# Optimization experiments

Hardware: AMD Instinct MI355X
Metric: run time of the kernel (lower is better)

## Reference

```python
import jax, jax.numpy as jnp
import numpy as np

B, CK, CQ, CV, CO, H, W = 4, 256, 256, 256, 64, 24, 24


def setup_inputs() -> dict:
    key = jax.random.key(0)
    ks = jax.random.split(key, 9)
    s = lambda k, shape, fan: jax.random.normal(k, shape, jnp.float32) * (fan ** -0.5)
    return {
        "key": jax.random.normal(ks[0], (B, CK, H, W), jnp.float32),
        "query": jax.random.normal(ks[1], (B, CQ, H, W), jnp.float32),
        "value": jax.random.normal(ks[2], (B, CV, H, W), jnp.float32),
        "Wk": s(ks[3], (CO, CK), CK),   # 1x1 conv weight for key transform
        "bk": jnp.zeros((CO,), jnp.float32),
        "Wq": s(ks[4], (CO, CQ), CQ),   # 1x1 conv weight for query transform
        "bq": jnp.zeros((CO,), jnp.float32),
        "wf": s(ks[5], (CO,), CO),      # channel-flattening 1x1 conv (CO -> 1)
        "bf": jnp.zeros((), jnp.float32),
    }


def reference(key, query, value, Wk, bk, Wq, bq, wf, bf):
    b, _, hq, wq = query.shape
    nk = key.shape[2] * key.shape[3]
    nq = hq * wq
    # 1x1 conv == per-pixel linear; flatten spatial to (B, N, CO)
    k_ = jnp.einsum('bchw,oc->bhwo', key, Wk).reshape(b, nk, -1) + bk
    q_ = jnp.einsum('bchw,oc->bhwo', query, Wq).reshape(b, nq, -1) + bq
    # broadcast add: (B, Nk, 1, CO) + (B, 1, Nq, CO) -> tanh -> reduce channels
    pre = jnp.tanh(k_[:, :, None, :] + q_[:, None, :, :])
    scores = jnp.einsum('bkqc,c->bkq', pre, wf) + bf
    attn = jax.nn.sigmoid(scores)                      # (B, Nk, Nq)
    v_ = value.reshape(b, value.shape[1], nk)          # (B, CV, Nk)
    out = jnp.einsum('bkq,bck->bcq', attn, v_)         # (B, CV, Nq)
    return out.reshape(b, value.shape[1], hq, wq)
```

## Files before the change

### kernel.cpp

```cpp
#include <hip/hip_runtime.h>
#include <hip/hip_bf16.h>

#define BB 4
#define CIN 256
#define CO 64
#define NN 576
#define NKC 18
#define NMT 36
#define NQT 36

typedef __attribute__((ext_vector_type(8))) short short8;
typedef __attribute__((ext_vector_type(4))) float floatx4;

__device__ __forceinline__ unsigned short f2bf(float f) {
    unsigned int u = __float_as_uint(f);
    unsigned int r = (u + 0x7fffu + ((u >> 16) & 1u)) >> 16;
    return (unsigned short)r;
}

__global__ void __launch_bounds__(256) pack_all(
    const float* __restrict__ key, const float* __restrict__ query,
    const float* __restrict__ value,
    const float* __restrict__ Wk, const float* __restrict__ Wq,
    unsigned short* __restrict__ Xp, unsigned short* __restrict__ Wp,
    unsigned short* __restrict__ Vp)
{
    __shared__ float tile[32][33];
    int bid = blockIdx.x;
    int t = threadIdx.x;
    int l = t & 63;
    int w = t >> 6;

    if (bid < 1152) {
        int zb  = bid / 144;
        int r   = bid % 144;
        int n32 = r % 18;
        int kc  = r / 18;
        int z = zb >> 2, b = zb & 3;
        const float* src = z ? query : key;
        int tx = t & 31, ty = t >> 5;
        const float* s = src + ((size_t)b * CIN + (size_t)kc * 32) * NN + n32 * 32;
        #pragma unroll
        for (int j = 0; j < 4; ++j) {
            int cl = ty + j * 8;
            tile[cl][tx] = s[(size_t)cl * NN + tx];
        }
        __syncthreads();
        if (w < 2) {
            int nl = w * 16 + (l & 15);
            int cl = (l >> 4) * 8;
            uint4 o;
            o.x = (unsigned)f2bf(tile[cl + 0][nl]) | ((unsigned)f2bf(tile[cl + 1][nl]) << 16);
            o.y = (unsigned)f2bf(tile[cl + 2][nl]) | ((unsigned)f2bf(tile[cl + 3][nl]) << 16);
            o.z = (unsigned)f2bf(tile[cl + 4][nl]) | ((unsigned)f2bf(tile[cl + 5][nl]) << 16);
            o.w = (unsigned)f2bf(tile[cl + 6][nl]) | ((unsigned)f2bf(tile[cl + 7][nl]) << 16);
            int mt = n32 * 2 + w;
            *(uint4*)(Xp + ((((size_t)z * BB + b) * NMT + mt) * 8 + kc) * 512 + l * 8) = o;
        }
    } else if (bid < 1168) {
        int funit = (bid - 1152) * 4 + w;
        int z  = funit >> 5;
        int nt = (funit >> 3) & 3;
        int kc = funit & 7;
        const float* W = z ? Wq : Wk;
        int o = nt * 16 + (l & 15);
        int c = kc * 32 + (l >> 4) * 8;
        const float4* p = (const float4*)(W + (size_t)o * CIN + c);
        float4 v0 = p[0], v1 = p[1];
        uint4 u;
        u.x = (unsigned)f2bf(v0.x) | ((unsigned)f2bf(v0.y) << 16);
        u.y = (unsigned)f2bf(v0.z) | ((unsigned)f2bf(v0.w) << 16);
        u.z = (unsigned)f2bf(v1.x) | ((unsigned)f2bf(v1.y) << 16);
        u.w = (unsigned)f2bf(v1.z) | ((unsigned)f2bf(v1.w) << 16);
        *(uint4*)(Wp + (((size_t)z * 4 + nt) * 8 + kc) * 512 + l * 8) = u;
    } else {
        int funit = (bid - 1168) * 4 + w;
        int b  = funit / 288;
        int r  = funit % 288;
        int ct = r / 18;
        int kc = r % 18;
        int c = ct * 16 + (l & 15);
        int k = kc * 32 + (l >> 4) * 8;
        const float4* p = (const float4*)(value + ((size_t)b * CIN + c) * NN + k);
        float4 v0 = p[0], v1 = p[1];
        uint4 u;
        u.x = (unsigned)f2bf(v0.x) | ((unsigned)f2bf(v0.y) << 16);
        u.y = (unsigned)f2bf(v0.z) | ((unsigned)f2bf(v0.w) << 16);
        u.z = (unsigned)f2bf(v1.x) | ((unsigned)f2bf(v1.y) << 16);
        u.w = (unsigned)f2bf(v1.z) | ((unsigned)f2bf(v1.w) << 16);
        *(uint4*)(Vp + (((size_t)b * 16 + ct) * NKC + kc) * 512 + l * 8) = u;
    }
}

__global__ void __launch_bounds__(256) proj_exp_mfma(
    const unsigned short* __restrict__ Xp, const unsigned short* __restrict__ Wp,
    const float* __restrict__ bk, const float* __restrict__ bq,
    float* __restrict__ ek, float* __restrict__ eq)
{
    int t = threadIdx.x, l = t & 63, w = t >> 6;
    int gw = blockIdx.x * 4 + w;
    int z  = gw / 144;
    int r  = gw % 144;
    int b  = r / NMT;
    int mt = r % NMT;

    const unsigned short* ab = Xp + ((((size_t)z * BB + b) * NMT + mt) * 8) * 512 + l * 8;
    const unsigned short* wb = Wp + (size_t)z * 32 * 512 + l * 8;

    floatx4 acc[4] = {{0.f,0.f,0.f,0.f},{0.f,0.f,0.f,0.f},
                      {0.f,0.f,0.f,0.f},{0.f,0.f,0.f,0.f}};
    #pragma unroll
    for (int kc = 0; kc < 8; ++kc) {
        short8 a = *(const short8*)(ab + (size_t)kc * 512);
        #pragma unroll
        for (int nt = 0; nt < 4; ++nt) {
            short8 bf8 = *(const short8*)(wb + ((size_t)nt * 8 + kc) * 512);
            acc[nt] = __builtin_amdgcn_mfma_f32_16x16x32_bf16(a, bf8, acc[nt], 0, 0, 0);
        }
    }

    const float* bias = z ? bq : bk;
    float* outp       = z ? eq : ek;
    int n0 = mt * 16;
    #pragma unroll
    for (int nt = 0; nt < 4; ++nt) {
        int o = nt * 16 + (l & 15);
        float bv = bias[o];
        #pragma unroll
        for (int rr = 0; rr < 4; ++rr) {
            int row = (l >> 4) * 4 + rr;
            outp[((size_t)b * NN + n0 + row) * CO + o] = __expf(2.0f * (acc[nt][rr] + bv));
        }
    }
}

__global__ void __launch_bounds__(256, 3) attn_pack_kernel(
    const float* __restrict__ ek, const float* __restrict__ eq,
    const float* __restrict__ wf, const float* __restrict__ bfp,
    unsigned short* __restrict__ Bp)
{
    int b  = blockIdx.z;
    int k0 = blockIdx.y * 32;
    int q0 = blockIdx.x * 64;
    int t  = threadIdx.x;
    int l  = t & 63;
    int w  = __builtin_amdgcn_readfirstlane(t >> 6);

    __shared__ float eqs[64 * 65];
    __shared__ float sc[32 * 65];

    const float4* esrc = (const float4*)(eq + ((size_t)b * NN + q0) * CO);
    #pragma unroll
    for (int i = 0; i < 4; ++i) {
        int f4  = t + i * 256;
        int row = f4 >> 4, c4 = (f4 & 15) * 4;
        float4 v = esrc[f4];
        int a = row * 65 + c4;
        eqs[a + 0] = v.x; eqs[a + 1] = v.y; eqs[a + 2] = v.z; eqs[a + 3] = v.w;
    }

    float4 w2v[16];
    float C = bfp[0];
    const float4* wfp4 = (const float4*)wf;
    #pragma unroll
    for (int i = 0; i < 16; ++i) {
        float4 wv = wfp4[i];
        C += wv.x + wv.y + wv.z + wv.w;
        wv.x *= 2.0f; wv.y *= 2.0f; wv.z *= 2.0f; wv.w *= 2.0f;
        w2v[i] = wv;
    }
    __syncthreads();

    float4 eqv[16];
    #pragma unroll
    for (int i = 0; i < 16; ++i) {
        int a = l * 65 + i * 4;
        eqv[i].x = eqs[a]; eqv[i].y = eqs[a + 1];
        eqv[i].z = eqs[a + 2]; eqv[i].w = eqs[a + 3];
    }

    #pragma unroll 1
    for (int kk = 0; kk < 8; ++kk) {
        int k = k0 + w * 8 + kk;
        const float4* ekr = (const float4*)(ek + ((size_t)b * NN + k) * CO);
        float a0 = 0.f, a1 = 0.f, a2 = 0.f, a3 = 0.f;
        #pragma unroll
        for (int i = 0; i < 16; ++i) {
            float4 k4 = ekr[i];
            float4 e4 = eqv[i];
            float4 w4 = w2v[i];
            a0 = fmaf(w4.x, __builtin_amdgcn_rcpf(fmaf(k4.x, e4.x, 1.0f)), a0);
            a1 = fmaf(w4.y, __builtin_amdgcn_rcpf(fmaf(k4.y, e4.y, 1.0f)), a1);
            a2 = fmaf(w4.z, __builtin_amdgcn_rcpf(fmaf(k4.z, e4.z, 1.0f)), a2);
            a3 = fmaf(w4.w, __builtin_amdgcn_rcpf(fmaf(k4.w, e4.w, 1.0f)), a3);
        }
        float score = C - (a0 + a1) - (a2 + a3);
        float sg = __builtin_amdgcn_rcpf(1.0f + __expf(-score));
        sc[(w * 8 + kk) * 65 + l] = sg;
    }
    __syncthreads();

    int col = w * 16 + (l & 15);
    int row = (l >> 4) * 8;
    uint4 o;
    o.x = (unsigned)f2bf(sc[(row + 0) * 65 + col]) | ((unsigned)f2bf(sc[(row + 1) * 65 + col]) << 16);
    o.y = (unsigned)f2bf(sc[(row + 2) * 65 + col]) | ((unsigned)f2bf(sc[(row + 3) * 65 + col]) << 16);
    o.z = (unsigned)f2bf(sc[(row + 4) * 65 + col]) | ((unsigned)f2bf(sc[(row + 5) * 65 + col]) << 16);
    o.w = (unsigned)f2bf(sc[(row + 6) * 65 + col]) | ((unsigned)f2bf(sc[(row + 7) * 65 + col]) << 16);
    size_t qt = (size_t)blockIdx.x * 4 + w;
    *(uint4*)(Bp + (((size_t)b * NQT + qt) * NKC + blockIdx.y) * 512 + l * 8) = o;
}

__global__ void __launch_bounds__(256) av_mfma_kernel(
    const unsigned short* __restrict__ Vp,
    const unsigned short* __restrict__ Bp,
    float* __restrict__ out)
{
    int b  = blockIdx.z;
    int ct = blockIdx.y;
    int qx = blockIdx.x;
    int t  = threadIdx.x;
    int l  = t & 63;
    int w  = __builtin_amdgcn_readfirstlane(t >> 6);

    floatx4 acc[4] = {{0.f,0.f,0.f,0.f},{0.f,0.f,0.f,0.f},
                      {0.f,0.f,0.f,0.f},{0.f,0.f,0.f,0.f}};

    const unsigned short* abase = Vp + ((size_t)b * 16 + ct) * NKC * 512 + l * 8;
    const unsigned short* bbase = Bp + ((size_t)b * NQT + (size_t)qx * 4) * NKC * 512 + l * 8;

    for (int kc = w; kc < NKC; kc += 4) {
        short8 a = *(const short8*)(abase + (size_t)kc * 512);
        #pragma unroll
        for (int qt = 0; qt < 4; ++qt) {
            short8 bq = *(const short8*)(bbase + ((size_t)qt * NKC + kc) * 512);
            acc[qt] = __builtin_amdgcn_mfma_f32_16x16x32_bf16(a, bq, acc[qt], 0, 0, 0);
        }
    }

    __shared__ float red[4][64][17];
    #pragma unroll
    for (int qt = 0; qt < 4; ++qt)
        #pragma unroll
        for (int r = 0; r < 4; ++r)
            red[w][l][qt * 4 + r] = acc[qt][r];
    __syncthreads();

    int q = qx * 64 + w * 16 + (l & 15);
    #pragma unroll
    for (int r = 0; r < 4; ++r) {
        float s = red[0][l][w * 4 + r] + red[1][l][w * 4 + r]
                + red[2][l][w * 4 + r] + red[3][l][w * 4 + r];
        int c = ct * 16 + (l >> 4) * 4 + r;
        out[((size_t)b * CIN + c) * NN + q] = s;
    }
}

extern "C" void kernel_launch(void* const* d_in, const int* in_sizes, int n_in,
                              void* d_out, int out_size, void* d_ws, size_t ws_size,
                              hipStream_t stream) {
    const float* key   = (const float*)d_in[0];
    const float* query = (const float*)d_in[1];
    const float* value = (const float*)d_in[2];
    const float* Wk    = (const float*)d_in[3];
    const float* bk    = (const float*)d_in[4];
    const float* Wq    = (const float*)d_in[5];
    const float* bq    = (const float*)d_in[6];
    const float* wf    = (const float*)d_in[7];
    const float* bf    = (const float*)d_in[8];
    float* out = (float*)d_out;

    float* ws = (float*)d_ws;
    float* ek = ws;
    float* eq = ek + (size_t)BB * NN * CO;
    unsigned short* Xp = (unsigned short*)(eq + (size_t)BB * NN * CO);
    unsigned short* Wp = Xp + (size_t)2 * BB * NMT * 8 * 512;
    unsigned short* Vp = Wp + (size_t)2 * 4 * 8 * 512;
    unsigned short* Bp = Vp + (size_t)BB * 16 * NKC * 512;

    pack_all<<<1456, 256, 0, stream>>>(key, query, value, Wk, Wq, Xp, Wp, Vp);

    proj_exp_mfma<<<72, 256, 0, stream>>>(Xp, Wp, bk, bq, ek, eq);

    dim3 ga(NN / 64, NN / 32, BB);
    attn_pack_kernel<<<ga, 256, 0, stream>>>(ek, eq, wf, bf, Bp);

    dim3 gm(NN / 64, 16, BB);
    av_mfma_kernel<<<gm, 256, 0, stream>>>(Vp, Bp, out);
}
```

Baseline: 102.3 us.

## Fuse input packing into projection MFMA kernel and stage ek tile in LDS

Merges the packing kernel and the projection MFMA kernel into one prep kernel. Each block now computes a 16-pixel projection tile directly from fp32 inputs, splitting K across four waves and reducing through LDS, which removes the bf16 Xp/Wp staging buffers and one launch. The attention kernel now stages its ek rows and the doubled wf weights in LDS and computes the bias constant with a wave reduction instead of per-thread register arrays, and its occupancy hint rises from 3 to 4 blocks. In exchange the prep kernel reads the weights redundantly per block, and the attention kernel uses more shared memory.

```diff
diff --git a/kernel.cpp b/kernel.cpp
--- a/kernel.cpp
+++ b/kernel.cpp
@@ -6,7 +6,6 @@
 #define CO 64
 #define NN 576
 #define NKC 18
-#define NMT 36
 #define NQT 36
 
 typedef __attribute__((ext_vector_type(8))) short short8;
@@ -18,67 +17,92 @@
     return (unsigned short)r;
 }
 
-__global__ void __launch_bounds__(256) pack_all(
+__global__ void __launch_bounds__(256) prep_kernel(
     const float* __restrict__ key, const float* __restrict__ query,
     const float* __restrict__ value,
     const float* __restrict__ Wk, const float* __restrict__ Wq,
-    unsigned short* __restrict__ Xp, unsigned short* __restrict__ Wp,
+    const float* __restrict__ bk, const float* __restrict__ bq,
+    float* __restrict__ ek, float* __restrict__ eq,
     unsigned short* __restrict__ Vp)
 {
-    __shared__ float tile[32][33];
+    __shared__ float red[4][4][64][4];
+    __shared__ float ex[16 * 69];
+
     int bid = blockIdx.x;
     int t = threadIdx.x;
     int l = t & 63;
-    int w = t >> 6;
-
-    if (bid < 1152) {
-        int zb  = bid / 144;
-        int r   = bid % 144;
-        int n32 = r % 18;
-        int kc  = r / 18;
-        int z = zb >> 2, b = zb & 3;
-        const float* src = z ? query : key;
-        int tx = t & 31, ty = t >> 5;
-        const float* s = src + ((size_t)b * CIN + (size_t)kc * 32) * NN + n32 * 32;
-        #pragma unroll
-        for (int j = 0; j < 4; ++j) {
-            int cl = ty + j * 8;
-            tile[cl][tx] = s[(size_t)cl * NN + tx];
-        }
+    int w = __builtin_amdgcn_readfirstlane(t >> 6);
+
+    if (bid < 288) {
+        int z  = bid / 144;
+        int r  = bid % 144;
+        int b  = r / 36;
+        int nt = r % 36;
+        int n0 = nt * 16;
+        const float* x = z ? query : key;
+        const float* W = z ? Wq : Wk;
+
+        floatx4 acc[4] = {{0.f,0.f,0.f,0.f},{0.f,0.f,0.f,0.f},
+                          {0.f,0.f,0.f,0.f},{0.f,0.f,0.f,0.f}};
+
+        #pragma unroll
+        for (int kci = 0; kci < 2; ++kci) {
+            int kc = w + kci * 4;
+            int cbase = kc * 32 + (l >> 4) * 8;
+            const float* xp = x + ((size_t)b * CIN + cbase) * NN + n0 + (l & 15);
+            uint4 bu;
+            {
+                float x0 = xp[0 * NN], x1 = xp[1 * NN], x2 = xp[2 * NN], x3 = xp[3 * NN];
+                float x4 = xp[4 * NN], x5 = xp[5 * NN], x6 = xp[6 * NN], x7 = xp[7 * NN];
+                bu.x = (unsigned)f2bf(x0) | ((unsigned)f2bf(x1) << 16);
+                bu.y = (unsigned)f2bf(x2) | ((unsigned)f2bf(x3) << 16);
+                bu.z = (unsigned)f2bf(x4) | ((unsigned)f2bf(x5) << 16);
+                bu.w = (unsigned)f2bf(x6) | ((unsigned)f2bf(x7) << 16);
+            }
+            short8 bx = *(short8*)&bu;
+            #pragma unroll
+            for (int mt = 0; mt < 4; ++mt) {
+                const float4* wp = (const float4*)(W + (size_t)(mt * 16 + (l & 15)) * CIN + cbase);
+                float4 w0 = wp[0], w1 = wp[1];
+                uint4 au;
+                au.x = (unsigned)f2bf(w0.x) | ((unsigned)f2bf(w0.y) << 16);
+                au.y = (unsigned)f2bf(w0.z) | ((unsigned)f2bf(w0.w) << 16);
+                au.z = (unsigned)f2bf(w1.x) | ((unsigned)f2bf(w1.y) << 16);
+                au.w = (unsigned)f2bf(w1.z) | ((unsigned)f2bf(w1.w) << 16);
+                acc[mt] = __builtin_amdgcn_mfma_f32_16x16x32_bf16(*(short8*)&au, bx, acc[mt], 0, 0, 0);
+            }
+        }
+        #pragma unroll
+        for (int mt = 0; mt < 4; ++mt)
+            #pragma unroll
+            for (int rr = 0; rr < 4; ++rr)
+                red[w][mt][l][rr] = acc[mt][rr];
         __syncthreads();
-        if (w < 2) {
-            int nl = w * 16 + (l & 15);
-            int cl = (l >> 4) * 8;
-            uint4 o;
-            o.x = (unsigned)f2bf(tile[cl + 0][nl]) | ((unsigned)f2bf(tile[cl + 1][nl]) << 16);
-            o.y = (unsigned)f2bf(tile[cl + 2][nl]) | ((unsigned)f2bf(tile[cl + 3][nl]) << 16);
-            o.z = (unsigned)f2bf(tile[cl + 4][nl]) | ((unsigned)f2bf(tile[cl + 5][nl]) << 16);
-            o.w = (unsigned)f2bf(tile[cl + 6][nl]) | ((unsigned)f2bf(tile[cl + 7][nl]) << 16);
-            int mt = n32 * 2 + w;
-            *(uint4*)(Xp + ((((size_t)z * BB + b) * NMT + mt) * 8 + kc) * 512 + l * 8) = o;
-        }
-    } else if (bid < 1168) {
-        int funit = (bid - 1152) * 4 + w;
-        int z  = funit >> 5;
-        int nt = (funit >> 3) & 3;
-        int kc = funit & 7;
-        const float* W = z ? Wq : Wk;
-        int o = nt * 16 + (l & 15);
-        int c = kc * 32 + (l >> 4) * 8;
-        const float4* p = (const float4*)(W + (size_t)o * CIN + c);
-        float4 v0 = p[0], v1 = p[1];
-        uint4 u;
-        u.x = (unsigned)f2bf(v0.x) | ((unsigned)f2bf(v0.y) << 16);
-        u.y = (unsigned)f2bf(v0.z) | ((unsigned)f2bf(v0.w) << 16);
-        u.z = (unsigned)f2bf(v1.x) | ((unsigned)f2bf(v1.y) << 16);
-        u.w = (unsigned)f2bf(v1.z) | ((unsigned)f2bf(v1.w) << 16);
-        *(uint4*)(Wp + (((size_t)z * 4 + nt) * 8 + kc) * 512 + l * 8) = u;
+
+        const float* bias = z ? bq : bk;
+        #pragma unroll
+        for (int rr = 0; rr < 4; ++rr) {
+            float v = red[0][w][l][rr] + red[1][w][l][rr]
+                    + red[2][w][l][rr] + red[3][w][l][rr];
+            int o = w * 16 + (l >> 4) * 4 + rr;
+            ex[(l & 15) * 69 + o] = __expf(2.0f * (v + bias[o]));
+        }
+        __syncthreads();
+
+        float* outp = z ? eq : ek;
+        float* obase = outp + ((size_t)b * NN + n0) * CO;
+        #pragma unroll
+        for (int i = 0; i < 4; ++i) {
+            int idx = t + i * 256;
+            int n = idx >> 6, o = idx & 63;
+            obase[(size_t)n * CO + o] = ex[n * 69 + o];
+        }
     } else {
-        int funit = (bid - 1168) * 4 + w;
+        int funit = (bid - 288) * 4 + w;
         int b  = funit / 288;
-        int r  = funit % 288;
-        int ct = r / 18;
-        int kc = r % 18;
+        int r2 = funit % 288;
+        int ct = r2 / NKC;
+        int kc = r2 % NKC;
         int c = ct * 16 + (l & 15);
         int k = kc * 32 + (l >> 4) * 8;
         const float4* p = (const float4*)(value + ((size_t)b * CIN + c) * NN + k);
@@ -92,49 +116,7 @@
     }
 }
 
-__global__ void __launch_bounds__(256) proj_exp_mfma(
-    const unsigned short* __restrict__ Xp, const unsigned short* __restrict__ Wp,
-    const float* __restrict__ bk, const float* __restrict__ bq,
-    float* __restrict__ ek, float* __restrict__ eq)
-{
-    int t = threadIdx.x, l = t & 63, w = t >> 6;
-    int gw = blockIdx.x * 4 + w;
-    int z  = gw / 144;
-    int r  = gw % 144;
-    int b  = r / NMT;
-    int mt = r % NMT;
-
-    const unsigned short* ab = Xp + ((((size_t)z * BB + b) * NMT + mt) * 8) * 512 + l * 8;
-    const unsigned short* wb = Wp + (size_t)z * 32 * 512 + l * 8;
-
-    floatx4 acc[4] = {{0.f,0.f,0.f,0.f},{0.f,0.f,0.f,0.f},
-                      {0.f,0.f,0.f,0.f},{0.f,0.f,0.f,0.f}};
-    #pragma unroll
-    for (int kc = 0; kc < 8; ++kc) {
-        short8 a = *(const short8*)(ab + (size_t)kc * 512);
-        #pragma unroll
-        for (int nt = 0; nt < 4; ++nt) {
-            short8 bf8 = *(const short8*)(wb + ((size_t)nt * 8 + kc) * 512);
-            acc[nt] = __builtin_amdgcn_mfma_f32_16x16x32_bf16(a, bf8, acc[nt], 0, 0, 0);
-        }
-    }
-
-    const float* bias = z ? bq : bk;
-    float* outp       = z ? eq : ek;
-    int n0 = mt * 16;
-    #pragma unroll
-    for (int nt = 0; nt < 4; ++nt) {
-        int o = nt * 16 + (l & 15);
-        float bv = bias[o];
-        #pragma unroll
-        for (int rr = 0; rr < 4; ++rr) {
-            int row = (l >> 4) * 4 + rr;
-            outp[((size_t)b * NN + n0 + row) * CO + o] = __expf(2.0f * (acc[nt][rr] + bv));
-        }
-    }
-}
-
-__global__ void __launch_bounds__(256, 3) attn_pack_kernel(
+__global__ void __launch_bounds__(256, 4) attn_pack_kernel(
     const float* __restrict__ ek, const float* __restrict__ eq,
     const float* __restrict__ wf, const float* __restrict__ bfp,
     unsigned short* __restrict__ Bp)
@@ -147,30 +129,37 @@
     int w  = __builtin_amdgcn_readfirstlane(t >> 6);
 
     __shared__ float eqs[64 * 65];
+    __shared__ float eks[32 * 68];
+    __shared__ float w2s[64];
+    __shared__ float Cs;
     __shared__ float sc[32 * 65];
 
     const float4* esrc = (const float4*)(eq + ((size_t)b * NN + q0) * CO);
     #pragma unroll
     for (int i = 0; i < 4; ++i) {
-        int f4  = t + i * 256;
+        int f4 = t + i * 256;
         int row = f4 >> 4, c4 = (f4 & 15) * 4;
         float4 v = esrc[f4];
         int a = row * 65 + c4;
-        eqs[a + 0] = v.x; eqs[a + 1] = v.y; eqs[a + 2] = v.z; eqs[a + 3] = v.w;
-    }
-
-    float4 w2v[16];
-    float C = bfp[0];
-    const float4* wfp4 = (const float4*)wf;
-    #pragma unroll
-    for (int i = 0; i < 16; ++i) {
-        float4 wv = wfp4[i];
-        C += wv.x + wv.y + wv.z + wv.w;
-        wv.x *= 2.0f; wv.y *= 2.0f; wv.z *= 2.0f; wv.w *= 2.0f;
-        w2v[i] = wv;
+        eqs[a] = v.x; eqs[a + 1] = v.y; eqs[a + 2] = v.z; eqs[a + 3] = v.w;
+    }
+    const float4* ksrc = (const float4*)(ek + ((size_t)b * NN + k0) * CO);
+    #pragma unroll
+    for (int i = 0; i < 2; ++i) {
+        int f4 = t + i * 256;
+        int row = f4 >> 4, c4 = (f4 & 15) * 4;
+        *(float4*)&eks[row * 68 + c4] = ksrc[f4];
+    }
+    if (t < 64) {
+        float v = wf[t];
+        w2s[t] = 2.0f * v;
+        #pragma unroll
+        for (int s = 32; s; s >>= 1) v += __shfl_xor(v, s, 64);
+        if (t == 0) Cs = v + bfp[0];
     }
     __syncthreads();
 
+    float C = Cs;
     float4 eqv[16];
     #pragma unroll
     for (int i = 0; i < 16; ++i) {
@@ -181,14 +170,14 @@
 
     #pragma unroll 1
     for (int kk = 0; kk < 8; ++kk) {
-        int k = k0 + w * 8 + kk;
-        const float4* ekr = (const float4*)(ek + ((size_t)b * NN + k) * CO);
+        int krow = w * 8 + kk;
+        const float* ekr = &eks[krow * 68];
         float a0 = 0.f, a1 = 0.f, a2 = 0.f, a3 = 0.f;
         #pragma unroll
         for (int i = 0; i < 16; ++i) {
-            float4 k4 = ekr[i];
+            float4 k4 = *(const float4*)(ekr + i * 4);
+            float4 w4 = *(const float4*)&w2s[i * 4];
             float4 e4 = eqv[i];
-            float4 w4 = w2v[i];
             a0 = fmaf(w4.x, __builtin_amdgcn_rcpf(fmaf(k4.x, e4.x, 1.0f)), a0);
             a1 = fmaf(w4.y, __builtin_amdgcn_rcpf(fmaf(k4.y, e4.y, 1.0f)), a1);
             a2 = fmaf(w4.z, __builtin_amdgcn_rcpf(fmaf(k4.z, e4.z, 1.0f)), a2);
@@ -196,7 +185,7 @@
         }
         float score = C - (a0 + a1) - (a2 + a3);
         float sg = __builtin_amdgcn_rcpf(1.0f + __expf(-score));
-        sc[(w * 8 + kk) * 65 + l] = sg;
+        sc[krow * 65 + l] = sg;
     }
     __syncthreads();
 
@@ -273,14 +262,10 @@
     float* ws = (float*)d_ws;
     float* ek = ws;
     float* eq = ek + (size_t)BB * NN * CO;
-    unsigned short* Xp = (unsigned short*)(eq + (size_t)BB * NN * CO);
-    unsigned short* Wp = Xp + (size_t)2 * BB * NMT * 8 * 512;
-    unsigned short* Vp = Wp + (size_t)2 * 4 * 8 * 512;
+    unsigned short* Vp = (unsigned short*)(eq + (size_t)BB * NN * CO);
     unsigned short* Bp = Vp + (size_t)BB * 16 * NKC * 512;
 
-    pack_all<<<1456, 256, 0, stream>>>(key, query, value, Wk, Wq, Xp, Wp, Vp);
-
-    proj_exp_mfma<<<72, 256, 0, stream>>>(Xp, Wp, bk, bq, ek, eq);
+    prep_kernel<<<576, 256, 0, stream>>>(key, query, value, Wk, Wq, bk, bq, ek, eq, Vp);
 
     dim3 ga(NN / 64, NN / 32, BB);
     attn_pack_kernel<<<ga, 256, 0, stream>>>(ek, eq, wf, bf, Bp);
```

New measurement: 174.4 us. +70.4%, slower.

## Stage ek tile and wf in LDS, widen pack tiles, split projection to one wave per block

Applied to the files above, without the earlier changes.

The attention kernel now loads its 32 ek rows and the doubled wf weights into shared memory once per block, and computes the wf sum with a wave shuffle reduction. Previously each wave read ek rows straight from global memory inside the inner loop and every thread kept wf in 16 float4 registers. The pack kernel transposes 64x32 tiles with all four waves writing output, where before it used 32x32 tiles with only two of four waves writing, so far fewer blocks are launched. The projection kernel runs one 64-thread wave per block over 288 blocks, spreading the work across more CUs. The extra LDS use in the attention kernel could lower occupancy, and reading w2s from LDS adds LDS traffic in the hot loop.

```diff
diff --git a/kernel.cpp b/kernel.cpp
--- a/kernel.cpp
+++ b/kernel.cpp
@@ -18,47 +18,58 @@
     return (unsigned short)r;
 }
 
-__global__ void __launch_bounds__(256) pack_all(
+__global__ void __launch_bounds__(256) pack_kernel(
     const float* __restrict__ key, const float* __restrict__ query,
     const float* __restrict__ value,
     const float* __restrict__ Wk, const float* __restrict__ Wq,
     unsigned short* __restrict__ Xp, unsigned short* __restrict__ Wp,
     unsigned short* __restrict__ Vp)
 {
-    __shared__ float tile[32][33];
+    __shared__ float tile[64 * 33];
     int bid = blockIdx.x;
-    int t = threadIdx.x;
-    int l = t & 63;
-    int w = t >> 6;
-
-    if (bid < 1152) {
-        int zb  = bid / 144;
-        int r   = bid % 144;
-        int n32 = r % 18;
-        int kc  = r / 18;
-        int z = zb >> 2, b = zb & 3;
-        const float* src = z ? query : key;
-        int tx = t & 31, ty = t >> 5;
-        const float* s = src + ((size_t)b * CIN + (size_t)kc * 32) * NN + n32 * 32;
-        #pragma unroll
-        for (int j = 0; j < 4; ++j) {
-            int cl = ty + j * 8;
-            tile[cl][tx] = s[(size_t)cl * NN + tx];
+    int t = threadIdx.x, l = t & 63, w = t >> 6;
+
+    if (bid < 576) {
+        int z = bid / 288, rem = bid % 288;
+        int b = rem / 72, rem2 = rem % 72;
+        int n32 = rem2 / 4, c64 = rem2 % 4;
+        const float* x = z ? query : key;
+        const float* s = x + ((size_t)b * CIN + c64 * 64) * NN + n32 * 32;
+        #pragma unroll
+        for (int j = 0; j < 8; ++j) {
+            int row = (t >> 5) + j * 8;
+            tile[row * 33 + (t & 31)] = s[(size_t)row * NN + (t & 31)];
         }
         __syncthreads();
-        if (w < 2) {
-            int nl = w * 16 + (l & 15);
-            int cl = (l >> 4) * 8;
-            uint4 o;
-            o.x = (unsigned)f2bf(tile[cl + 0][nl]) | ((unsigned)f2bf(tile[cl + 1][nl]) << 16);
-            o.y = (unsigned)f2bf(tile[cl + 2][nl]) | ((unsigned)f2bf(tile[cl + 3][nl]) << 16);
-            o.z = (unsigned)f2bf(tile[cl + 4][nl]) | ((unsigned)f2bf(tile[cl + 5][nl]) << 16);
-            o.w = (unsigned)f2bf(tile[cl + 6][nl]) | ((unsigned)f2bf(tile[cl + 7][nl]) << 16);
-            int mt = n32 * 2 + w;
-            *(uint4*)(Xp + ((((size_t)z * BB + b) * NMT + mt) * 8 + kc) * 512 + l * 8) = o;
-        }
-    } else if (bid < 1168) {
-        int funit = (bid - 1152) * 4 + w;
+        int mtl = w & 1, kcl = w >> 1;
+        int nl = mtl * 16 + (l & 15);
+        int cl = kcl * 32 + (l >> 4) * 8;
+        uint4 o;
+        o.x = (unsigned)f2bf(tile[(cl + 0) * 33 + nl]) | ((unsigned)f2bf(tile[(cl + 1) * 33 + nl]) << 16);
+        o.y = (unsigned)f2bf(tile[(cl + 2) * 33 + nl]) | ((unsigned)f2bf(tile[(cl + 3) * 33 + nl]) << 16);
+        o.z = (unsigned)f2bf(tile[(cl + 4) * 33 + nl]) | ((unsigned)f2bf(tile[(cl + 5) * 33 + nl]) << 16);
+        o.w = (unsigned)f2bf(tile[(cl + 6) * 33 + nl]) | ((unsigned)f2bf(tile[(cl + 7) * 33 + nl]) << 16);
+        int mt = n32 * 2 + mtl;
+        int kc = c64 * 2 + kcl;
+        *(uint4*)(Xp + ((((size_t)z * BB + b) * NMT + mt) * 8 + kc) * 512 + l * 8) = o;
+    } else if (bid < 864) {
+        int funit = (bid - 576) * 4 + w;
+        int b  = funit / 288;
+        int r2 = funit % 288;
+        int ct = r2 / NKC;
+        int kc = r2 % NKC;
+        int c = ct * 16 + (l & 15);
+        int k = kc * 32 + (l >> 4) * 8;
+        const float4* p = (const float4*)(value + ((size_t)b * CIN + c) * NN + k);
+        float4 v0 = p[0], v1 = p[1];
+        uint4 u;
+        u.x = (unsigned)f2bf(v0.x) | ((unsigned)f2bf(v0.y) << 16);
+        u.y = (unsigned)f2bf(v0.z) | ((unsigned)f2bf(v0.w) << 16);
+        u.z = (unsigned)f2bf(v1.x) | ((unsigned)f2bf(v1.y) << 16);
+        u.w = (unsigned)f2bf(v1.z) | ((unsigned)f2bf(v1.w) << 16);
+        *(uint4*)(Vp + (((size_t)b * 16 + ct) * NKC + kc) * 512 + l * 8) = u;
+    } else {
+        int funit = (bid - 864) * 4 + w;
         int z  = funit >> 5;
         int nt = (funit >> 3) & 3;
         int kc = funit & 7;
@@ -73,32 +84,16 @@
         u.z = (unsigned)f2bf(v1.x) | ((unsigned)f2bf(v1.y) << 16);
         u.w = (unsigned)f2bf(v1.z) | ((unsigned)f2bf(v1.w) << 16);
         *(uint4*)(Wp + (((size_t)z * 4 + nt) * 8 + kc) * 512 + l * 8) = u;
-    } else {
-        int funit = (bid - 1168) * 4 + w;
-        int b  = funit / 288;
-        int r  = funit % 288;
-        int ct = r / 18;
-        int kc = r % 18;
-        int c = ct * 16 + (l & 15);
-        int k = kc * 32 + (l >> 4) * 8;
-        const float4* p = (const float4*)(value + ((size_t)b * CIN + c) * NN + k);
-        float4 v0 = p[0], v1 = p[1];
-        uint4 u;
-        u.x = (unsigned)f2bf(v0.x) | ((unsigned)f2bf(v0.y) << 16);
-        u.y = (unsigned)f2bf(v0.z) | ((unsigned)f2bf(v0.w) << 16);
-        u.z = (unsigned)f2bf(v1.x) | ((unsigned)f2bf(v1.y) << 16);
-        u.w = (unsigned)f2bf(v1.z) | ((unsigned)f2bf(v1.w) << 16);
-        *(uint4*)(Vp + (((size_t)b * 16 + ct) * NKC + kc) * 512 + l * 8) = u;
-    }
-}
-
-__global__ void __launch_bounds__(256) proj_exp_mfma(
+    }
+}
+
+__global__ void __launch_bounds__(64) proj_exp_mfma(
     const unsigned short* __restrict__ Xp, const unsigned short* __restrict__ Wp,
     const float* __restrict__ bk, const float* __restrict__ bq,
     float* __restrict__ ek, float* __restrict__ eq)
 {
-    int t = threadIdx.x, l = t & 63, w = t >> 6;
-    int gw = blockIdx.x * 4 + w;
+    int l = threadIdx.x;
+    int gw = blockIdx.x;
     int z  = gw / 144;
     int r  = gw % 144;
     int b  = r / NMT;
@@ -114,8 +109,8 @@
         short8 a = *(const short8*)(ab + (size_t)kc * 512);
         #pragma unroll
         for (int nt = 0; nt < 4; ++nt) {
-            short8 bf8 = *(const short8*)(wb + ((size_t)nt * 8 + kc) * 512);
-            acc[nt] = __builtin_amdgcn_mfma_f32_16x16x32_bf16(a, bf8, acc[nt], 0, 0, 0);
+            short8 bw = *(const short8*)(wb + ((size_t)nt * 8 + kc) * 512);
+            acc[nt] = __builtin_amdgcn_mfma_f32_16x16x32_bf16(a, bw, acc[nt], 0, 0, 0);
         }
     }
 
@@ -147,30 +142,37 @@
     int w  = __builtin_amdgcn_readfirstlane(t >> 6);
 
     __shared__ float eqs[64 * 65];
+    __shared__ float eks[32 * 68];
+    __shared__ float w2s[64];
+    __shared__ float Cs;
     __shared__ float sc[32 * 65];
 
     const float4* esrc = (const float4*)(eq + ((size_t)b * NN + q0) * CO);
     #pragma unroll
     for (int i = 0; i < 4; ++i) {
-        int f4  = t + i * 256;
+        int f4 = t + i * 256;
         int row = f4 >> 4, c4 = (f4 & 15) * 4;
         float4 v = esrc[f4];
         int a = row * 65 + c4;
-        eqs[a + 0] = v.x; eqs[a + 1] = v.y; eqs[a + 2] = v.z; eqs[a + 3] = v.w;
-    }
-
-    float4 w2v[16];
-    float C = bfp[0];
-    const float4* wfp4 = (const float4*)wf;
-    #pragma unroll
-    for (int i = 0; i < 16; ++i) {
-        float4 wv = wfp4[i];
-        C += wv.x + wv.y + wv.z + wv.w;
-        wv.x *= 2.0f; wv.y *= 2.0f; wv.z *= 2.0f; wv.w *= 2.0f;
-        w2v[i] = wv;
+        eqs[a] = v.x; eqs[a + 1] = v.y; eqs[a + 2] = v.z; eqs[a + 3] = v.w;
+    }
+    const float4* ksrc = (const float4*)(ek + ((size_t)b * NN + k0) * CO);
+    #pragma unroll
+    for (int i = 0; i < 2; ++i) {
+        int f4 = t + i * 256;
+        int row = f4 >> 4, c4 = (f4 & 15) * 4;
+        *(float4*)&eks[row * 68 + c4] = ksrc[f4];
+    }
+    if (t < 64) {
+        float v = wf[t];
+        w2s[t] = 2.0f * v;
+        #pragma unroll
+        for (int s = 32; s; s >>= 1) v += __shfl_xor(v, s, 64);
+        if (t == 0) Cs = v + bfp[0];
     }
     __syncthreads();
 
+    float C = Cs;
     float4 eqv[16];
     #pragma unroll
     for (int i = 0; i < 16; ++i) {
@@ -181,14 +183,14 @@
 
     #pragma unroll 1
     for (int kk = 0; kk < 8; ++kk) {
-        int k = k0 + w * 8 + kk;
-        const float4* ekr = (const float4*)(ek + ((size_t)b * NN + k) * CO);
+        int krow = w * 8 + kk;
+        const float* ekr = &eks[krow * 68];
         float a0 = 0.f, a1 = 0.f, a2 = 0.f, a3 = 0.f;
         #pragma unroll
         for (int i = 0; i < 16; ++i) {
-            float4 k4 = ekr[i];
+            float4 k4 = *(const float4*)(ekr + i * 4);
+            float4 w4 = *(const float4*)&w2s[i * 4];
             float4 e4 = eqv[i];
-            float4 w4 = w2v[i];
             a0 = fmaf(w4.x, __builtin_amdgcn_rcpf(fmaf(k4.x, e4.x, 1.0f)), a0);
             a1 = fmaf(w4.y, __builtin_amdgcn_rcpf(fmaf(k4.y, e4.y, 1.0f)), a1);
             a2 = fmaf(w4.z, __builtin_amdgcn_rcpf(fmaf(k4.z, e4.z, 1.0f)), a2);
@@ -196,7 +198,7 @@
         }
         float score = C - (a0 + a1) - (a2 + a3);
         float sg = __builtin_amdgcn_rcpf(1.0f + __expf(-score));
-        sc[(w * 8 + kk) * 65 + l] = sg;
+        sc[krow * 65 + l] = sg;
     }
     __syncthreads();
 
@@ -278,9 +280,9 @@
     unsigned short* Vp = Wp + (size_t)2 * 4 * 8 * 512;
     unsigned short* Bp = Vp + (size_t)BB * 16 * NKC * 512;
 
-    pack_all<<<1456, 256, 0, stream>>>(key, query, value, Wk, Wq, Xp, Wp, Vp);
-
-    proj_exp_mfma<<<72, 256, 0, stream>>>(Xp, Wp, bk, bq, ek, eq);
+    pack_kernel<<<880, 256, 0, stream>>>(key, query, value, Wk, Wq, Xp, Wp, Vp);
+
+    proj_exp_mfma<<<288, 64, 0, stream>>>(Xp, Wp, bk, bq, ek, eq);
 
     dim3 ga(NN / 64, NN / 32, BB);
     attn_pack_kernel<<<ga, 256, 0, stream>>>(ek, eq, wf, bf, Bp);
```

After: 111.3 us. +8.7%, slower.
